# Kernel optimization log

Hardware: AMD Instinct MI355X
Metric: run time of the kernel (lower is better)

Reference implementation:

```python
import jax, jax.numpy as jnp
from jax import lax
import numpy as np

TAU = 10.0
BN_EPS = 1e-5
M_CENTROIDS = 1024
K_NEIGHBORS = 32


def fps(xyz, m):
    """Farthest point sampling for a single cloud xyz:(N,3) -> (m,) int32 indices."""
    N = xyz.shape[0]

    def step(carry, _):
        dists, last = carry
        d = jnp.sum((xyz - xyz[last]) ** 2, axis=-1)  # (N,)
        dists = jnp.minimum(dists, d)
        nxt = jnp.argmax(dists).astype(jnp.int32)
        return (dists, nxt), nxt

    init = (jnp.full((N,), 1e10, xyz.dtype), jnp.int32(0))
    _, idxs = lax.scan(step, init, None, length=m - 1)
    return jnp.concatenate([jnp.zeros((1,), jnp.int32), idxs])


def conv_bn_relu(x, W, g, b):
    # 1x1 Conv2d (no bias) == channel matmul; BatchNorm in train mode (batch stats)
    x = jnp.einsum('bmkc,oc->bmko', x, W)
    mu = jnp.mean(x, axis=(0, 1, 2))
    var = jnp.var(x, axis=(0, 1, 2))  # biased, matching torch BN normalization
    return jax.nn.relu((x - mu) * (g * lax.rsqrt(var + BN_EPS)) + b)


def lse_pool(x, tau=TAU):
    # Log-Sum-Exp pool over K axis (axis=2) of (B,M,K,C)
    x_max = jnp.max(x, axis=2)
    return x_max + jnp.log(jnp.sum(jnp.exp(tau * (x - x_max[:, :, None, :])), axis=2)) / tau


def setup_inputs() -> dict:
    key = jax.random.key(0)
    ks = jax.random.split(key, 5)
    B, N, C = 16, 4096, 64
    return {
        'xyz': jax.random.normal(ks[0], (B, N, 3), jnp.float32),
        'features': jax.random.normal(ks[1], (B, N, C), jnp.float32),
        'W1': jax.random.normal(ks[2], (64, 67), jnp.float32) * 0.1,
        'g1': jnp.ones((64,), jnp.float32),
        'b1': jnp.zeros((64,), jnp.float32),
        'W2': jax.random.normal(ks[3], (64, 64), jnp.float32) * 0.1,
        'g2': jnp.ones((64,), jnp.float32),
        'b2': jnp.zeros((64,), jnp.float32),
        'W3': jax.random.normal(ks[4], (128, 64), jnp.float32) * 0.1,
        'g3': jnp.ones((128,), jnp.float32),
        'b3': jnp.zeros((128,), jnp.float32),
    }


def reference(xyz, features, W1, g1, b1, W2, g2, b2, W3, g3, b3):
    B, N, _ = xyz.shape
    M, K = M_CENTROIDS, K_NEIGHBORS
    # FPS (indices non-differentiable, as in torch_geometric fps)
    idx = jax.vmap(lambda p: fps(p, M))(xyz)  # (B,M)
    centroids = jnp.take_along_axis(xyz, idx[:, :, None], axis=1)  # (B,M,3)
    # KNN via pairwise squared distances (computed under no_grad in original)
    d2 = (jnp.sum(centroids ** 2, -1)[:, :, None]
          + jnp.sum(xyz ** 2, -1)[:, None, :]
          - 2.0 * jnp.einsum('bmc,bnc->bmn', centroids, xyz))  # (B,M,N)
    group_idx = lax.top_k(-lax.stop_gradient(d2), K)[1]  # (B,M,K)
    bidx = jnp.arange(B)[:, None, None]
    grouped_xyz = xyz[bidx, group_idx] - centroids[:, :, None, :]  # (B,M,K,3)
    grouped_feat = features[bidx, group_idx]  # (B,M,K,C)
    x = jnp.concatenate([grouped_xyz, grouped_feat], axis=-1)  # (B,M,K,3+C)
    x = conv_bn_relu(x, W1, g1, b1)
    x = conv_bn_relu(x, W2, g2, b2)
    x = conv_bn_relu(x, W3, g3, b3)
    x = lse_pool(x)  # (B,M,128)
    return (centroids, x)
```

## Files before the change

kernel.cpp:

```cpp
#include <hip/hip_runtime.h>
#include <math.h>

#define B_   16
#define N_   4096
#define M_   1024
#define K_   32
#define CIN  67
#define NPOS (B_*M_*K_)
#define NBLK (NPOS/128)
#define BN_EPS 1e-5f

typedef unsigned short ushort_t;
typedef unsigned long long u64_t;

__device__ __forceinline__ unsigned int pack2bf(float a, float b) {
    unsigned int ua = __float_as_uint(a); ua = (ua + 0x7fffu + ((ua >> 16) & 1u)) >> 16;
    unsigned int ub = __float_as_uint(b); ub = (ub + 0x7fffu + ((ub >> 16) & 1u)) >> 16;
    return ua | (ub << 16);
}
__device__ __forceinline__ void unpack2(unsigned int u, float& lo, float& hi) {
    lo = __uint_as_float(u << 16);
    hi = __uint_as_float(u & 0xffff0000u);
}

__global__ __launch_bounds__(256) void fps_kernel(const float* __restrict__ xyz,
                                                  float* __restrict__ cent)
{
    __shared__ float sx[N_], sy[N_], sz[N_];
    __shared__ __align__(16) float red[2][4][8];
    const int b = blockIdx.x;
    const int t = threadIdx.x;

    const float4* xf = (const float4*)(xyz + (size_t)b * (N_*3));
#pragma unroll
    for (int u0 = 0; u0 < 4; ++u0) {
        const int u = u0 * 256 + t;
        const float4 q0 = xf[3*u+0], q1 = xf[3*u+1], q2 = xf[3*u+2];
        sx[4*u+0] = q0.x; sx[4*u+1] = q0.w; sx[4*u+2] = q1.z; sx[4*u+3] = q2.y;
        sy[4*u+0] = q0.y; sy[4*u+1] = q1.x; sy[4*u+2] = q1.w; sy[4*u+3] = q2.z;
        sz[4*u+0] = q0.z; sz[4*u+1] = q1.y; sz[4*u+2] = q2.x; sz[4*u+3] = q2.w;
    }
    __syncthreads();

    float px[16], py[16], pz[16], dist[16];
    unsigned int nl[16];
#pragma unroll
    for (int s = 0; s < 16; ++s) {
        const int p = s * 256 + t;
        px[s] = sx[p]; py[s] = sy[p]; pz[s] = sz[p];
        dist[s] = 1e10f;
        nl[s] = ~(unsigned int)p;
    }

    float cx = sx[0], cy = sy[0], cz = sz[0];
    if (t == 0) {
        float* o = cent + (size_t)b * M_ * 3;
        o[0] = cx; o[1] = cy; o[2] = cz;
    }
    const int lane = t & 63, w = t >> 6;

#pragma unroll 1
    for (int i = 1; i < M_; ++i) {
        u64_t best = 0ull;
#pragma unroll
        for (int s = 0; s < 16; ++s) {
            const float dx = __fsub_rn(px[s], cx);
            const float dy = __fsub_rn(py[s], cy);
            const float dz = __fsub_rn(pz[s], cz);
            const float d  = __fadd_rn(__fadd_rn(__fmul_rn(dx,dx), __fmul_rn(dy,dy)),
                                       __fmul_rn(dz,dz));
            dist[s] = fminf(dist[s], d);
            const u64_t cand = ((u64_t)__float_as_uint(dist[s]) << 32) | nl[s];
            best = (cand > best) ? cand : best;
        }
#pragma unroll
        for (int off = 32; off >= 1; off >>= 1) {
            const u64_t o = __shfl_down(best, off);
            best = (o > best) ? o : best;
        }
        if (lane == 0) {
            const unsigned int p = ~(unsigned int)(best & 0xffffffffull);
            red[i&1][w][0] = __uint_as_float((unsigned int)(best >> 32));
            red[i&1][w][1] = __uint_as_float((unsigned int)(best & 0xffffffffull));
            red[i&1][w][2] = sx[p]; red[i&1][w][3] = sy[p]; red[i&1][w][4] = sz[p];
        }
        __syncthreads();
        u64_t kk[4]; float xx[4], yy[4], zz[4];
#pragma unroll
        for (int ww = 0; ww < 4; ++ww) {
            const float4 r = *(const float4*)&red[i&1][ww][0];
            kk[ww] = ((u64_t)__float_as_uint(r.x) << 32) | __float_as_uint(r.y);
            xx[ww] = r.z; yy[ww] = r.w; zz[ww] = red[i&1][ww][4];
        }
#define MERGE_(a, c_) { const bool s_ = kk[c_] > kk[a]; \
        kk[a] = s_ ? kk[c_] : kk[a]; xx[a] = s_ ? xx[c_] : xx[a]; \
        yy[a] = s_ ? yy[c_] : yy[a]; zz[a] = s_ ? zz[c_] : zz[a]; }
        MERGE_(0,1); MERGE_(2,3); MERGE_(0,2);
#undef MERGE_
        cx = xx[0]; cy = yy[0]; cz = zz[0];
        if (t == 0) {
            float* o = cent + ((size_t)b * M_ + i) * 3;
            o[0] = cx; o[1] = cy; o[2] = cz;
        }
    }
}

__global__ __launch_bounds__(1024) void knn_kernel(const float* __restrict__ xyz,
                                                   const float* __restrict__ cent,
                                                   int* __restrict__ gidx)
{
    __shared__ float sx[N_], sy[N_], sz[N_], sn[N_];
    const int b  = blockIdx.x >> 6;
    const int mg = blockIdx.x & 63;
    const int t  = threadIdx.x;
    {
        const float4* xf = (const float4*)(xyz + (size_t)b * (N_*3));
        float4 q0 = xf[3*t+0], q1 = xf[3*t+1], q2 = xf[3*t+2];
        float ax[4] = {q0.x, q0.w, q1.z, q2.y};
        float ay[4] = {q0.y, q1.x, q1.w, q2.z};
        float az[4] = {q0.z, q1.y, q2.x, q2.w};
#pragma unroll
        for (int j = 0; j < 4; ++j) {
            const int p = 4*t + j;
            sx[p] = ax[j]; sy[p] = ay[j]; sz[p] = az[j];
            sn[p] = __fadd_rn(__fadd_rn(__fmul_rn(ax[j],ax[j]), __fmul_rn(ay[j],ay[j])),
                              __fmul_rn(az[j],az[j]));
        }
    }
    __syncthreads();
    const int w = t >> 6, lane = t & 63;
    const int m = mg * 16 + w;
    const float* c = cent + ((size_t)b * M_ + m) * 3;
    const float cx = c[0], cy = c[1], cz = c[2];
    const float cn = __fadd_rn(__fadd_rn(__fmul_rn(cx,cx), __fmul_rn(cy,cy)),
                               __fmul_rn(cz,cz));
    unsigned int key[64];
    u64_t b1 = ~0ull, b2 = ~0ull;
#pragma unroll
    for (int j = 0; j < 64; ++j) {
        const int p = j*64 + lane;
        const float dot = __fadd_rn(__fadd_rn(__fmul_rn(cx,sx[p]), __fmul_rn(cy,sy[p])),
                                    __fmul_rn(cz,sz[p]));
        const float d = __fsub_rn(__fadd_rn(cn, sn[p]), __fmul_rn(2.0f, dot));
        const unsigned int bb = __float_as_uint(d);
        const unsigned int k = (bb & 0x80000000u) ? ~bb : (bb | 0x80000000u);
        key[j] = k;
        const u64_t cand = ((u64_t)k << 32) | (unsigned int)p;
        if (cand < b1) { b2 = b1; b1 = cand; } else if (cand < b2) { b2 = cand; }
    }
    u64_t used = 0ull;
    int* gout = gidx + ((size_t)b * M_ + m) * K_;
#pragma unroll 1
    for (int r = 0; r < K_; ++r) {
        u64_t v = b1;
#pragma unroll
        for (int off = 1; off < 64; off <<= 1) {
            const u64_t ov = __shfl_xor(v, off);
            v = (ov < v) ? ov : v;
        }
        if (lane == 0) gout[r] = (int)(v & 0xffffffffull);
        if (v == b1) {
            const int p = (int)(v & 0xffffffffull);
            used |= (1ull << (p >> 6));
            if (b2 != ~0ull) { b1 = b2; b2 = ~0ull; }
            else {
                b1 = ~0ull; b2 = ~0ull;
#pragma unroll
                for (int jj = 0; jj < 64; ++jj) {
                    if (!(used & (1ull << jj))) {
                        const u64_t cand = ((u64_t)key[jj] << 32) | (unsigned int)(jj*64 + lane);
                        if (cand < b1) { b2 = b1; b1 = cand; } else if (cand < b2) { b2 = cand; }
                    }
                }
            }
        }
    }
}

__device__ __forceinline__ void write_stats64(float acc[4][8], float* part,
                                              float (*sred)[128][2], int t, int blk,
                                              int obase)
{
    const int lane = t & 63, w = t >> 6;
    const int txl = lane & 7, tyl = lane >> 3;
    float s[8], q[8];
#pragma unroll
    for (int j = 0; j < 8; ++j) {
        s[j] = ((acc[0][j] + acc[1][j]) + acc[2][j]) + acc[3][j];
        q[j] = ((acc[0][j]*acc[0][j] + acc[1][j]*acc[1][j]) + acc[2][j]*acc[2][j])
               + acc[3][j]*acc[3][j];
    }
#pragma unroll
    for (int off = 8; off < 64; off <<= 1) {
#pragma unroll
        for (int j = 0; j < 8; ++j) {
            s[j] += __shfl_xor(s[j], off);
            q[j] += __shfl_xor(q[j], off);
        }
    }
    if (tyl == 0) {
#pragma unroll
        for (int j = 0; j < 8; ++j) { sred[w][txl*8+j][0] = s[j]; sred[w][txl*8+j][1] = q[j]; }
    }
    __syncthreads();
    if (t < 128) {
        const int o = t >> 1, which = t & 1;
        const float v = ((sred[0][o][which] + sred[1][o][which]) + sred[2][o][which])
                        + sred[3][o][which];
        part[(size_t)(which*128 + obase + o) * NBLK + blk] = v;
    }
}

__device__ __forceinline__ void write_stats128(float a3[8][8], float* part,
                                               float (*sred)[128][2], int t, int blk)
{
    const int lane = t & 63, w = t >> 6;
    const int txl = lane & 15, tyl = lane >> 4;
    float s[8], q[8];
#pragma unroll
    for (int j = 0; j < 8; ++j) {
        float ss0 = 0.f, qq0 = 0.f;
#pragma unroll
        for (int i = 0; i < 8; ++i) { ss0 += a3[i][j]; qq0 += a3[i][j]*a3[i][j]; }
        s[j] = ss0; q[j] = qq0;
    }
#pragma unroll
    for (int off = 16; off < 64; off <<= 1) {
#pragma unroll
        for (int j = 0; j < 8; ++j) {
            s[j] += __shfl_xor(s[j], off);
            q[j] += __shfl_xor(q[j], off);
        }
    }
    if (tyl == 0) {
#pragma unroll
        for (int j = 0; j < 8; ++j) { sred[w][txl*8+j][0] = s[j]; sred[w][txl*8+j][1] = q[j]; }
    }
    __syncthreads();
    {
        const int o = t >> 1, which = t & 1;
        const float v = ((sred[0][o][which] + sred[1][o][which]) + sred[2][o][which])
                        + sred[3][o][which];
        part[(size_t)(which*128 + o) * NBLK + blk] = v;
    }
}

__global__ __launch_bounds__(256) void passA_kernel(const float* __restrict__ xyz,
    const float* __restrict__ feat, const float* __restrict__ W1,
    const float* __restrict__ cent, const int* __restrict__ gidx,
    float* __restrict__ part, ushort_t* __restrict__ z1)
{
    __shared__ __align__(16) float buf[CIN][132];
    __shared__ __align__(16) float wb[64*68];
    __shared__ float sred[4][128][2];
    const int t = threadIdx.x;
    const int blk = blockIdx.x;
    const int pos0 = blk * 128;

    {
        const int ph = t >> 1, half = t & 1;
        const int pos = pos0 + ph;
        const int b = pos >> 15;
        const int n = gidx[pos];
        const float* fbase = feat + ((((size_t)b << 12) + (size_t)n) << 6) + (half << 5);
        const float4* fp4 = (const float4*)fbase;
#pragma unroll
        for (int q = 0; q < 8; ++q) {
            const float4 v = fp4[q];
            const int c = 3 + (half << 5) + (q << 2);
            buf[c+0][ph] = v.x; buf[c+1][ph] = v.y; buf[c+2][ph] = v.z; buf[c+3][ph] = v.w;
        }
        if (half == 0) {
            const int bm = pos >> 5;
            const float* pp = xyz + (((size_t)b << 12) + (size_t)n) * 3;
            const float* cc = cent + (size_t)bm * 3;
            buf[0][ph] = __fsub_rn(pp[0], cc[0]);
            buf[1][ph] = __fsub_rn(pp[1], cc[1]);
            buf[2][ph] = __fsub_rn(pp[2], cc[2]);
        }
        const int o = t & 63, chunk = t >> 6;
        const int c0 = chunk * 17;
        const int c1 = (c0 + 17 < CIN) ? (c0 + 17) : CIN;
        for (int c = c0; c < c1; ++c) wb[c*68 + o] = W1[o*CIN + c];
    }
    __syncthreads();

    const int tx = t & 7, ty = t >> 3;
    float acc[4][8];
#pragma unroll
    for (int i = 0; i < 4; ++i)
#pragma unroll
        for (int j = 0; j < 8; ++j) acc[i][j] = 0.0f;
#pragma unroll 1
    for (int c = 0; c < CIN; ++c) {
        const float4 xv = *(const float4*)&buf[c][ty*4];
        const float4 w0 = *(const float4*)&wb[c*68 + tx*8];
        const float4 w1 = *(const float4*)&wb[c*68 + tx*8 + 4];
        const float xs[4] = {xv.x, xv.y, xv.z, xv.w};
        const float wv[8] = {w0.x, w0.y, w0.z, w0.w, w1.x, w1.y, w1.z, w1.w};
#pragma unroll
        for (int i = 0; i < 4; ++i)
#pragma unroll
            for (int j = 0; j < 8; ++j) acc[i][j] = fmaf(xs[i], wv[j], acc[i][j]);
    }
    write_stats64(acc, part, sred, t, blk, 0);
#pragma unroll
    for (int i = 0; i < 4; ++i) {
        uint4 s;
        s.x = pack2bf(acc[i][0], acc[i][1]); s.y = pack2bf(acc[i][2], acc[i][3]);
        s.z = pack2bf(acc[i][4], acc[i][5]); s.w = pack2bf(acc[i][6], acc[i][7]);
        *(uint4*)(z1 + ((size_t)(pos0 + ty*4 + i)) * 64 + tx*8) = s;
    }
}

__global__ __launch_bounds__(256) void passB_kernel(const float* __restrict__ W2,
    const float* __restrict__ ss, const ushort_t* __restrict__ z1,
    float* __restrict__ part, ushort_t* __restrict__ z2)
{
    __shared__ __align__(16) float buf[64][132];
    __shared__ __align__(16) float wb[64*68];
    __shared__ float sred[4][128][2];
    __shared__ float ssl[64], ssh[64];
    const int t = threadIdx.x;
    const int blk = blockIdx.x;
    const int pos0 = blk * 128;

    if (t < 64) { ssl[t] = ss[t]; ssh[t] = ss[128 + t]; }
    {
        const int o = t & 63, chunk = t >> 6;
#pragma unroll
        for (int cc2 = 0; cc2 < 16; ++cc2) {
            const int c = chunk*16 + cc2;
            wb[c*68 + o] = W2[o*64 + c];
        }
    }
    __syncthreads();

    {
        const int ph = t >> 1, half = t & 1;
        const uint4* zr = (const uint4*)(z1 + ((size_t)(pos0 + ph)) * 64 + half*32);
#pragma unroll
        for (int q = 0; q < 4; ++q) {
            const uint4 r = zr[q];
            const int c = half*32 + q*8;
            float lo, hi;
            unpack2(r.x, lo, hi);
            buf[c+0][ph] = fmaxf(fmaf(lo, ssl[c+0], ssh[c+0]), 0.f);
            buf[c+1][ph] = fmaxf(fmaf(hi, ssl[c+1], ssh[c+1]), 0.f);
            unpack2(r.y, lo, hi);
            buf[c+2][ph] = fmaxf(fmaf(lo, ssl[c+2], ssh[c+2]), 0.f);
            buf[c+3][ph] = fmaxf(fmaf(hi, ssl[c+3], ssh[c+3]), 0.f);
            unpack2(r.z, lo, hi);
            buf[c+4][ph] = fmaxf(fmaf(lo, ssl[c+4], ssh[c+4]), 0.f);
            buf[c+5][ph] = fmaxf(fmaf(hi, ssl[c+5], ssh[c+5]), 0.f);
            unpack2(r.w, lo, hi);
            buf[c+6][ph] = fmaxf(fmaf(lo, ssl[c+6], ssh[c+6]), 0.f);
            buf[c+7][ph] = fmaxf(fmaf(hi, ssl[c+7], ssh[c+7]), 0.f);
        }
    }
    __syncthreads();

    const int tx = t & 7, ty = t >> 3;
    float acc[4][8];
#pragma unroll
    for (int i = 0; i < 4; ++i)
#pragma unroll
        for (int j = 0; j < 8; ++j) acc[i][j] = 0.0f;
#pragma unroll 1
    for (int c = 0; c < 64; ++c) {
        const float4 xv = *(const float4*)&buf[c][ty*4];
        const float4 w0 = *(const float4*)&wb[c*68 + tx*8];
        const float4 w1 = *(const float4*)&wb[c*68 + tx*8 + 4];
        const float xs[4] = {xv.x, xv.y, xv.z, xv.w};
        const float wv[8] = {w0.x, w0.y, w0.z, w0.w, w1.x, w1.y, w1.z, w1.w};
#pragma unroll
        for (int i = 0; i < 4; ++i)
#pragma unroll
            for (int j = 0; j < 8; ++j) acc[i][j] = fmaf(xs[i], wv[j], acc[i][j]);
    }
    write_stats64(acc, part, sred, t, blk, 0);
#pragma unroll
    for (int i = 0; i < 4; ++i) {
        uint4 s;
        s.x = pack2bf(acc[i][0], acc[i][1]); s.y = pack2bf(acc[i][2], acc[i][3]);
        s.z = pack2bf(acc[i][4], acc[i][5]); s.w = pack2bf(acc[i][6], acc[i][7]);
        *(uint4*)(z2 + ((size_t)(pos0 + ty*4 + i)) * 64 + tx*8) = s;
    }
}

__global__ __launch_bounds__(256) void passC_kernel(const float* __restrict__ W3,
    const float* __restrict__ ss, const ushort_t* __restrict__ z2,
    float* __restrict__ part, ushort_t* __restrict__ z3)
{
    __shared__ __align__(16) float buf[64][132];
    __shared__ __align__(16) float wb[64*68];
    __shared__ float sred[4][128][2];
    __shared__ float ssl[64], ssh[64];
    const int t = threadIdx.x;
    const int blk = blockIdx.x;
    const int pos0 = blk * 128;

    if (t < 64) { ssl[t] = ss[256 + t]; ssh[t] = ss[384 + t]; }
    {
        const int o = t & 63, chunk = t >> 6;
#pragma unroll
        for (int cc3 = 0; cc3 < 16; ++cc3) {
            const int c = chunk*16 + cc3;
            wb[c*68 + o] = W3[o*64 + c];
        }
    }
    __syncthreads();

    {
        const int ph = t >> 1, half = t & 1;
        const uint4* zr = (const uint4*)(z2 + ((size_t)(pos0 + ph)) * 64 + half*32);
#pragma unroll
        for (int q = 0; q < 4; ++q) {
            const uint4 r = zr[q];
            const int c = half*32 + q*8;
            float lo, hi;
            unpack2(r.x, lo, hi);
            buf[c+0][ph] = fmaxf(fmaf(lo, ssl[c+0], ssh[c+0]), 0.f);
            buf[c+1][ph] = fmaxf(fmaf(hi, ssl[c+1], ssh[c+1]), 0.f);
            unpack2(r.y, lo, hi);
            buf[c+2][ph] = fmaxf(fmaf(lo, ssl[c+2], ssh[c+2]), 0.f);
            buf[c+3][ph] = fmaxf(fmaf(hi, ssl[c+3], ssh[c+3]), 0.f);
            unpack2(r.z, lo, hi);
            buf[c+4][ph] = fmaxf(fmaf(lo, ssl[c+4], ssh[c+4]), 0.f);
            buf[c+5][ph] = fmaxf(fmaf(hi, ssl[c+5], ssh[c+5]), 0.f);
            unpack2(r.w, lo, hi);
            buf[c+6][ph] = fmaxf(fmaf(lo, ssl[c+6], ssh[c+6]), 0.f);
            buf[c+7][ph] = fmaxf(fmaf(hi, ssl[c+7], ssh[c+7]), 0.f);
        }
    }
    __syncthreads();

    const int tx = t & 7, ty = t >> 3;
#pragma unroll 1
    for (int h = 0; h < 2; ++h) {
        float acc[4][8];
#pragma unroll
        for (int i = 0; i < 4; ++i)
#pragma unroll
            for (int j = 0; j < 8; ++j) acc[i][j] = 0.0f;
#pragma unroll 1
        for (int c = 0; c < 64; ++c) {
            const float4 xv = *(const float4*)&buf[c][ty*4];
            const float4 w0 = *(const float4*)&wb[c*68 + tx*8];
            const float4 w1 = *(const float4*)&wb[c*68 + tx*8 + 4];
            const float xs[4] = {xv.x, xv.y, xv.z, xv.w};
            const float wv[8] = {w0.x, w0.y, w0.z, w0.w, w1.x, w1.y, w1.z, w1.w};
#pragma unroll
            for (int i = 0; i < 4; ++i)
#pragma unroll
                for (int j = 0; j < 8; ++j) acc[i][j] = fmaf(xv[i], wv[j], acc[i][j]);
        }
        write_stats64(acc, part, sred, t, blk, h*64);
#pragma unroll
        for (int i = 0; i < 4; ++i) {
            uint4 s;
            s.x = pack2bf(acc[i][0], acc[i][1]); s.y = pack2bf(acc[i][2], acc[i][3]);
            s.z = pack2bf(acc[i][4], acc[i][5]); s.w = pack2bf(acc[i][6], acc[i][7]);
            *(uint4*)(z3 + ((size_t)(pos0 + ty*4 + i)) * 128 + h*64 + tx*8) = s;
        }
        if (h == 0) {
            const int o = t & 63, chunk = t >> 6;
#pragma unroll
            for (int cc3 = 0; cc3 < 16; ++cc3) {
                const int c = chunk*16 + cc3;
                wb[c*68 + o] = W3[(64 + o)*64 + c];
            }
            __syncthreads();
        }
    }
}

__global__ __launch_bounds__(256) void passD_kernel(const float* __restrict__ ss,
    const ushort_t* __restrict__ z3, float* __restrict__ outx)
{
    const int t = threadIdx.x;
    const int blk = blockIdx.x;
    const int pos0 = blk * 128;
    const int tx3 = t & 15, ty3 = t >> 4;
    const int lane = t & 63, w = t >> 6;
    float scl[8], shf[8];
#pragma unroll
    for (int j = 0; j < 8; ++j) { scl[j] = ss[512 + tx3*8 + j]; shf[j] = ss[640 + tx3*8 + j]; }

    float v[8][8];
#pragma unroll
    for (int i = 0; i < 8; ++i) {
        const uint4 r = *(const uint4*)(z3 + ((size_t)(pos0 + ty3*8 + i)) * 128 + tx3*8);
        float lo, hi;
        unpack2(r.x, lo, hi);
        v[i][0] = fmaxf(fmaf(lo, scl[0], shf[0]), 0.f);
        v[i][1] = fmaxf(fmaf(hi, scl[1], shf[1]), 0.f);
        unpack2(r.y, lo, hi);
        v[i][2] = fmaxf(fmaf(lo, scl[2], shf[2]), 0.f);
        v[i][3] = fmaxf(fmaf(hi, scl[3], shf[3]), 0.f);
        unpack2(r.z, lo, hi);
        v[i][4] = fmaxf(fmaf(lo, scl[4], shf[4]), 0.f);
        v[i][5] = fmaxf(fmaf(hi, scl[5], shf[5]), 0.f);
        unpack2(r.w, lo, hi);
        v[i][6] = fmaxf(fmaf(lo, scl[6], shf[6]), 0.f);
        v[i][7] = fmaxf(fmaf(hi, scl[7], shf[7]), 0.f);
    }
    float mrow[8], srow[8];
#pragma unroll
    for (int j = 0; j < 8; ++j) {
        float mm = v[0][j];
#pragma unroll
        for (int i = 1; i < 8; ++i) mm = fmaxf(mm, v[i][j]);
        float sm = 0.0f;
#pragma unroll
        for (int i = 0; i < 8; ++i) sm += expf(10.0f * (v[i][j] - mm));
        mrow[j] = mm; srow[j] = sm;
    }
#pragma unroll
    for (int off = 16; off <= 32; off <<= 1) {
#pragma unroll
        for (int j = 0; j < 8; ++j) {
            const float om = __shfl_xor(mrow[j], off);
            const float os = __shfl_xor(srow[j], off);
            const float nm = fmaxf(mrow[j], om);
            srow[j] = srow[j] * expf(10.0f*(mrow[j]-nm)) + os * expf(10.0f*(om-nm));
            mrow[j] = nm;
        }
    }
    if ((lane >> 4) == 0) {
        const int bm = blk*4 + w;
#pragma unroll
        for (int j = 0; j < 8; ++j)
            outx[(size_t)bm*128 + tx3*8 + j] = mrow[j] + logf(srow[j]) / 10.0f;
    }
}

template<int PASS>
__global__ __launch_bounds__(256) void fwd_kernel(const float* __restrict__ xyz,
    const float* __restrict__ feat, const float* __restrict__ W1,
    const float* __restrict__ W2, const float* __restrict__ W3,
    const float* __restrict__ cent, const int* __restrict__ gidx,
    const float* __restrict__ ss, float* __restrict__ part, float* __restrict__ outx)
{
    __shared__ __align__(16) float buf[CIN][132];
    __shared__ __align__(16) float wb[64*132];
    __shared__ float sred[4][128][2];
    const int t = threadIdx.x;
    const int blk = blockIdx.x;
    const int pos0 = blk * 128;
    const int lane = t & 63, w = t >> 6;

    {
        const int ph = t >> 1, half = t & 1;
        const int pos = pos0 + ph;
        const int b = pos >> 15;
        const int n = gidx[pos];
        const float* fbase = feat + ((((size_t)b << 12) + (size_t)n) << 6) + (half << 5);
        const float4* fp4 = (const float4*)fbase;
#pragma unroll
        for (int q = 0; q < 8; ++q) {
            const float4 v = fp4[q];
            const int c = 3 + (half << 5) + (q << 2);
            buf[c+0][ph] = v.x; buf[c+1][ph] = v.y; buf[c+2][ph] = v.z; buf[c+3][ph] = v.w;
        }
        if (half == 0) {
            const int bm = pos >> 5;
            const float* pp = xyz + (((size_t)b << 12) + (size_t)n) * 3;
            const float* cc = cent + (size_t)bm * 3;
            buf[0][ph] = __fsub_rn(pp[0], cc[0]);
            buf[1][ph] = __fsub_rn(pp[1], cc[1]);
            buf[2][ph] = __fsub_rn(pp[2], cc[2]);
        }
        const int o = t & 63, chunk = t >> 6;
        const int c0 = chunk * 17;
        const int c1 = (c0 + 17 < CIN) ? (c0 + 17) : CIN;
        for (int c = c0; c < c1; ++c) wb[c*68 + o] = W1[o*CIN + c];
    }
    __syncthreads();

    const int tx = t & 7, ty = t >> 3;
    float acc[4][8];
#pragma unroll
    for (int i = 0; i < 4; ++i)
#pragma unroll
        for (int j = 0; j < 8; ++j) acc[i][j] = 0.0f;
#pragma unroll 1
    for (int c = 0; c < CIN; ++c) {
        const float4 xv = *(const float4*)&buf[c][ty*4];
        const float4 w0 = *(const float4*)&wb[c*68 + tx*8];
        const float4 w1 = *(const float4*)&wb[c*68 + tx*8 + 4];
        const float xs[4] = {xv.x, xv.y, xv.z, xv.w};
        const float wv[8] = {w0.x, w0.y, w0.z, w0.w, w1.x, w1.y, w1.z, w1.w};
#pragma unroll
        for (int i = 0; i < 4; ++i)
#pragma unroll
            for (int j = 0; j < 8; ++j) acc[i][j] = fmaf(xs[i], wv[j], acc[i][j]);
    }
    if (PASS == 1) { write_stats64(acc, part, sred, t, blk, 0); return; }

    __syncthreads();
    {
        float scl[8], shf[8];
#pragma unroll
        for (int j = 0; j < 8; ++j) { scl[j] = ss[tx*8+j]; shf[j] = ss[128 + tx*8+j]; }
#pragma unroll
        for (int jj = 0; jj < 8; ++jj) {
            const int j = (tx + jj) & 7;
#pragma unroll
            for (int i = 0; i < 4; ++i)
                buf[tx*8+j][ty*4+i] = fmaxf(fmaf(acc[i][j], scl[j], shf[j]), 0.0f);
        }
        const int o = t & 63, chunk = t >> 6;
#pragma unroll
        for (int cc2 = 0; cc2 < 16; ++cc2) {
            const int c = chunk*16 + cc2;
            wb[c*68 + o] = W2[o*64 + c];
        }
    }
    __syncthreads();

#pragma unroll
    for (int i = 0; i < 4; ++i)
#pragma unroll
        for (int j = 0; j < 8; ++j) acc[i][j] = 0.0f;
#pragma unroll 1
    for (int c = 0; c < 64; ++c) {
        const float4 xv = *(const float4*)&buf[c][ty*4];
        const float4 w0 = *(const float4*)&wb[c*68 + tx*8];
        const float4 w1 = *(const float4*)&wb[c*68 + tx*8 + 4];
        const float xs[4] = {xv.x, xv.y, xv.z, xv.w};
        const float wv[8] = {w0.x, w0.y, w0.z, w0.w, w1.x, w1.y, w1.z, w1.w};
#pragma unroll
        for (int i = 0; i < 4; ++i)
#pragma unroll
            for (int j = 0; j < 8; ++j) acc[i][j] = fmaf(xs[i], wv[j], acc[i][j]);
    }
    if (PASS == 2) { write_stats64(acc, part, sred, t, blk, 0); return; }

    __syncthreads();
    {
        float scl[8], shf[8];
#pragma unroll
        for (int j = 0; j < 8; ++j) { scl[j] = ss[256 + tx*8+j]; shf[j] = ss[256 + 128 + tx*8+j]; }
#pragma unroll
        for (int jj = 0; jj < 8; ++jj) {
            const int j = (tx + jj) & 7;
#pragma unroll
            for (int i = 0; i < 4; ++i)
                buf[tx*8+j][ty*4+i] = fmaxf(fmaf(acc[i][j], scl[j], shf[j]), 0.0f);
        }
        const int o = t & 127, chunk = t >> 7;
#pragma unroll
        for (int cc3 = 0; cc3 < 32; ++cc3) {
            const int c = chunk*32 + cc3;
            wb[c*132 + o] = W3[o*64 + c];
        }
    }
    __syncthreads();

    const int tx3 = t & 15, ty3 = t >> 4;
    float a3[8][8];
#pragma unroll
    for (int i = 0; i < 8; ++i)
#pragma unroll
        for (int j = 0; j < 8; ++j) a3[i][j] = 0.0f;
#pragma unroll 1
    for (int c = 0; c < 64; ++c) {
        const float4 x0 = *(const float4*)&buf[c][ty3*8];
        const float4 x1 = *(const float4*)&buf[c][ty3*8 + 4];
        const float4 w0 = *(const float4*)&wb[c*132 + tx3*8];
        const float4 w1 = *(const float4*)&wb[c*132 + tx3*8 + 4];
        const float xs[8] = {x0.x, x0.y, x0.z, x0.w, x1.x, x1.y, x1.z, x1.w};
        const float wv[8] = {w0.x, w0.y, w0.z, w0.w, w1.x, w1.y, w1.z, w1.w};
#pragma unroll
        for (int i = 0; i < 8; ++i)
#pragma unroll
            for (int j = 0; j < 8; ++j) a3[i][j] = fmaf(xs[i], wv[j], a3[i][j]);
    }
    if (PASS == 3) { write_stats128(a3, part, sred, t, blk); return; }

    {
        float scl[8], shf[8];
#pragma unroll
        for (int j = 0; j < 8; ++j) { scl[j] = ss[512 + tx3*8+j]; shf[j] = ss[512 + 128 + tx3*8+j]; }
        float mrow[8], srow[8];
#pragma unroll
        for (int j = 0; j < 8; ++j) {
            float vv[8];
#pragma unroll
            for (int i = 0; i < 8; ++i)
                vv[i] = fmaxf(fmaf(a3[i][j], scl[j], shf[j]), 0.0f);
            float mm = vv[0];
#pragma unroll
            for (int i = 1; i < 8; ++i) mm = fmaxf(mm, vv[i]);
            float sm = 0.0f;
#pragma unroll
            for (int i = 0; i < 8; ++i) sm += expf(10.0f * (vv[i] - mm));
            mrow[j] = mm; srow[j] = sm;
        }
#pragma unroll
        for (int off = 16; off <= 32; off <<= 1) {
#pragma unroll
            for (int j = 0; j < 8; ++j) {
                const float om = __shfl_xor(mrow[j], off);
                const float os = __shfl_xor(srow[j], off);
                const float nm = fmaxf(mrow[j], om);
                srow[j] = srow[j] * expf(10.0f*(mrow[j]-nm)) + os * expf(10.0f*(om-nm));
                mrow[j] = nm;
            }
        }
        if ((lane >> 4) == 0) {
            const int bm = blk*4 + w;
#pragma unroll
            for (int j = 0; j < 8; ++j)
                outx[(size_t)bm*128 + tx3*8 + j] = mrow[j] + logf(srow[j]) / 10.0f;
        }
    }
}

__global__ __launch_bounds__(256) void stats_kernel(const float* __restrict__ part,
    const float* __restrict__ g, const float* __restrict__ bet,
    float* __restrict__ ss, int si)
{
    __shared__ float red[512];
    const int o = blockIdx.x, t = threadIdx.x;
    const float* ps = part + (size_t)o * NBLK;
    const float* pq = part + (size_t)(128 + o) * NBLK;
    float s = 0.0f, q = 0.0f;
    for (int i = t; i < NBLK; i += 256) { s += ps[i]; q += pq[i]; }
    red[t] = s; red[256 + t] = q;
    __syncthreads();
    for (int st = 128; st > 0; st >>= 1) {
        if (t < st) { red[t] += red[t + st]; red[256+t] += red[256+t+st]; }
        __syncthreads();
    }
    if (t == 0) {
        const float inv = 1.0f / (float)NPOS;
        const float mu  = red[0] * inv;
        const float var = red[256] * inv - mu * mu;
        const float scale = g[o] / sqrtf(var + BN_EPS);
        ss[si*256 + o]       = scale;
        ss[si*256 + 128 + o] = bet[o] - mu * scale;
    }
}

extern "C" void kernel_launch(void* const* d_in, const int* in_sizes, int n_in,
                              void* d_out, int out_size, void* d_ws, size_t ws_size,
                              hipStream_t stream) {
    const float* xyz  = (const float*)d_in[0];
    const float* feat = (const float*)d_in[1];
    const float* W1   = (const float*)d_in[2];
    const float* g1   = (const float*)d_in[3];
    const float* b1   = (const float*)d_in[4];
    const float* W2   = (const float*)d_in[5];
    const float* g2   = (const float*)d_in[6];
    const float* b2   = (const float*)d_in[7];
    const float* W3   = (const float*)d_in[8];
    const float* g3   = (const float*)d_in[9];
    const float* b3   = (const float*)d_in[10];
    float* out = (float*)d_out;
    float* wsf = (float*)d_ws;

    float* part = wsf;
    int*   gidx = (int*)(wsf + 2*128*NBLK);
    float* ss   = wsf + 2*128*NBLK + NPOS;
    float* outx = out + B_*M_*3;

    const size_t BASE0 = (size_t)(2*128*NBLK + NPOS + 768) * 4;
    const size_t ZA_BYTES = (size_t)NPOS * 128 * 2;
    const size_t ZB_BYTES = (size_t)NPOS * 64 * 2;
    const size_t NEED = BASE0 + ZA_BYTES + ZB_BYTES;
    ushort_t* zA = (ushort_t*)((char*)d_ws + BASE0);
    ushort_t* zB = (ushort_t*)((char*)d_ws + BASE0 + ZA_BYTES);

    fps_kernel<<<dim3(B_), dim3(256), 0, stream>>>(xyz, out);
    knn_kernel<<<dim3(B_*64), dim3(1024), 0, stream>>>(xyz, out, gidx);

    if (ws_size >= NEED) {
        passA_kernel<<<dim3(NBLK), dim3(256), 0, stream>>>(xyz, feat, W1, out, gidx, part, zA);
        stats_kernel<<<dim3(64), dim3(256), 0, stream>>>(part, g1, b1, ss, 0);
        passB_kernel<<<dim3(NBLK), dim3(256), 0, stream>>>(W2, ss, zA, part, zB);
        stats_kernel<<<dim3(64), dim3(256), 0, stream>>>(part, g2, b2, ss, 1);
        passC_kernel<<<dim3(NBLK), dim3(256), 0, stream>>>(W3, ss, zB, part, zA);
        stats_kernel<<<dim3(128), dim3(256), 0, stream>>>(part, g3, b3, ss, 2);
        passD_kernel<<<dim3(NBLK), dim3(256), 0, stream>>>(ss, zA, outx);
    } else {
        fwd_kernel<1><<<dim3(NBLK), dim3(256), 0, stream>>>(xyz, feat, W1, W2, W3, out, gidx, ss, part, outx);
        stats_kernel<<<dim3(64), dim3(256), 0, stream>>>(part, g1, b1, ss, 0);
        fwd_kernel<2><<<dim3(NBLK), dim3(256), 0, stream>>>(xyz, feat, W1, W2, W3, out, gidx, ss, part, outx);
        stats_kernel<<<dim3(64), dim3(256), 0, stream>>>(part, g2, b2, ss, 1);
        fwd_kernel<3><<<dim3(NBLK), dim3(256), 0, stream>>>(xyz, feat, W1, W2, W3, out, gidx, ss, part, outx);
        stats_kernel<<<dim3(128), dim3(256), 0, stream>>>(part, g3, b3, ss, 2);
        fwd_kernel<4><<<dim3(NBLK), dim3(256), 0, stream>>>(xyz, feat, W1, W2, W3, out, gidx, ss, part, outx);
    }
}
```

Before: 1.666 ms.

## Precompute per-point feature projection and overlap it with FPS blocks

The first 1x1 conv is split algebraically. The 64 feature channels are projected once per input point (B*N points instead of B*M*K grouped positions), and only the 3 relative-xyz channels are applied per neighbour in passA, which gathers the precomputed rows. That projection runs as extra blocks inside the FPS launch so it overlaps the long serial FPS loop. FPS now reduces only indices per step and writes centroids at the end, and passC computes all 128 outputs in one pass with a padded weight tile. The fp32 projected buffer reuses the zB workspace, and the larger shared-memory footprint of the combined kernel may reduce occupancy.

Result: faster. 1.483 ms (-11.0%).

```diff
diff --git a/kernel.cpp b/kernel.cpp
--- a/kernel.cpp
+++ b/kernel.cpp
@@ -23,84 +23,126 @@
     hi = __uint_as_float(u & 0xffff0000u);
 }
 
-__global__ __launch_bounds__(256) void fps_kernel(const float* __restrict__ xyz,
-                                                  float* __restrict__ cent)
+__global__ __launch_bounds__(256) void fps_a0_kernel(const float* __restrict__ xyz,
+    float* __restrict__ cent, const float* __restrict__ feat,
+    const float* __restrict__ W1, float* __restrict__ z1u)
 {
     __shared__ float sx[N_], sy[N_], sz[N_];
-    __shared__ __align__(16) float red[2][4][8];
-    const int b = blockIdx.x;
+    __shared__ u64_t red[2][4];
+    __shared__ int cidx[M_];
+    __shared__ __align__(16) float buf[64][132];
+    __shared__ __align__(16) float wb[64*68];
+
     const int t = threadIdx.x;
 
-    const float4* xf = (const float4*)(xyz + (size_t)b * (N_*3));
-#pragma unroll
-    for (int u0 = 0; u0 < 4; ++u0) {
-        const int u = u0 * 256 + t;
-        const float4 q0 = xf[3*u+0], q1 = xf[3*u+1], q2 = xf[3*u+2];
-        sx[4*u+0] = q0.x; sx[4*u+1] = q0.w; sx[4*u+2] = q1.z; sx[4*u+3] = q2.y;
-        sy[4*u+0] = q0.y; sy[4*u+1] = q1.x; sy[4*u+2] = q1.w; sy[4*u+3] = q2.z;
-        sz[4*u+0] = q0.z; sz[4*u+1] = q1.y; sz[4*u+2] = q2.x; sz[4*u+3] = q2.w;
-    }
-    __syncthreads();
-
-    float px[16], py[16], pz[16], dist[16];
-    unsigned int nl[16];
-#pragma unroll
-    for (int s = 0; s < 16; ++s) {
-        const int p = s * 256 + t;
-        px[s] = sx[p]; py[s] = sy[p]; pz[s] = sz[p];
-        dist[s] = 1e10f;
-        nl[s] = ~(unsigned int)p;
-    }
-
-    float cx = sx[0], cy = sy[0], cz = sz[0];
-    if (t == 0) {
-        float* o = cent + (size_t)b * M_ * 3;
-        o[0] = cx; o[1] = cy; o[2] = cz;
-    }
-    const int lane = t & 63, w = t >> 6;
-
+    if (blockIdx.x < 16) {
+        const int b = blockIdx.x;
+        const float4* xf = (const float4*)(xyz + (size_t)b * (N_*3));
+#pragma unroll
+        for (int u0 = 0; u0 < 4; ++u0) {
+            const int u = u0 * 256 + t;
+            const float4 q0 = xf[3*u+0], q1 = xf[3*u+1], q2 = xf[3*u+2];
+            sx[4*u+0] = q0.x; sx[4*u+1] = q0.w; sx[4*u+2] = q1.z; sx[4*u+3] = q2.y;
+            sy[4*u+0] = q0.y; sy[4*u+1] = q1.x; sy[4*u+2] = q1.w; sy[4*u+3] = q2.z;
+            sz[4*u+0] = q0.z; sz[4*u+1] = q1.y; sz[4*u+2] = q2.x; sz[4*u+3] = q2.w;
+        }
+        if (t == 0) cidx[0] = 0;
+        __syncthreads();
+
+        float px[16], py[16], pz[16], dist[16];
+        unsigned int nl[16];
+#pragma unroll
+        for (int s = 0; s < 16; ++s) {
+            const int p = s * 256 + t;
+            px[s] = sx[p]; py[s] = sy[p]; pz[s] = sz[p];
+            dist[s] = 1e10f;
+            nl[s] = ~(unsigned int)p;
+        }
+
+        int last = 0;
 #pragma unroll 1
-    for (int i = 1; i < M_; ++i) {
-        u64_t best = 0ull;
-#pragma unroll
-        for (int s = 0; s < 16; ++s) {
-            const float dx = __fsub_rn(px[s], cx);
-            const float dy = __fsub_rn(py[s], cy);
-            const float dz = __fsub_rn(pz[s], cz);
-            const float d  = __fadd_rn(__fadd_rn(__fmul_rn(dx,dx), __fmul_rn(dy,dy)),
-                                       __fmul_rn(dz,dz));
-            dist[s] = fminf(dist[s], d);
-            const u64_t cand = ((u64_t)__float_as_uint(dist[s]) << 32) | nl[s];
-            best = (cand > best) ? cand : best;
-        }
-#pragma unroll
-        for (int off = 32; off >= 1; off >>= 1) {
-            const u64_t o = __shfl_down(best, off);
-            best = (o > best) ? o : best;
-        }
-        if (lane == 0) {
-            const unsigned int p = ~(unsigned int)(best & 0xffffffffull);
-            red[i&1][w][0] = __uint_as_float((unsigned int)(best >> 32));
-            red[i&1][w][1] = __uint_as_float((unsigned int)(best & 0xffffffffull));
-            red[i&1][w][2] = sx[p]; red[i&1][w][3] = sy[p]; red[i&1][w][4] = sz[p];
+        for (int i = 1; i < M_; ++i) {
+            const float cx = sx[last], cy = sy[last], cz = sz[last];
+            u64_t best = 0ull;
+#pragma unroll
+            for (int s = 0; s < 16; ++s) {
+                const float dx = __fsub_rn(px[s], cx);
+                const float dy = __fsub_rn(py[s], cy);
+                const float dz = __fsub_rn(pz[s], cz);
+                const float d  = __fadd_rn(__fadd_rn(__fmul_rn(dx,dx), __fmul_rn(dy,dy)),
+                                           __fmul_rn(dz,dz));
+                dist[s] = fminf(dist[s], d);
+                const u64_t cand = ((u64_t)__float_as_uint(dist[s]) << 32) | nl[s];
+                best = (cand > best) ? cand : best;
+            }
+#pragma unroll
+            for (int off = 1; off < 64; off <<= 1) {
+                const u64_t o = __shfl_xor(best, off);
+                best = (o > best) ? o : best;
+            }
+            if ((t & 63) == 0) red[i & 1][t >> 6] = best;
+            __syncthreads();
+            const u64_t g0 = red[i&1][0], g1 = red[i&1][1];
+            const u64_t g2 = red[i&1][2], g3 = red[i&1][3];
+            const u64_t ga = (g0 > g1) ? g0 : g1;
+            const u64_t gb = (g2 > g3) ? g2 : g3;
+            const u64_t g  = (ga > gb) ? ga : gb;
+            last = (int)(~(unsigned int)g);
+            if (t == 0) cidx[i] = last;
         }
         __syncthreads();
-        u64_t kk[4]; float xx[4], yy[4], zz[4];
-#pragma unroll
-        for (int ww = 0; ww < 4; ++ww) {
-            const float4 r = *(const float4*)&red[i&1][ww][0];
-            kk[ww] = ((u64_t)__float_as_uint(r.x) << 32) | __float_as_uint(r.y);
-            xx[ww] = r.z; yy[ww] = r.w; zz[ww] = red[i&1][ww][4];
-        }
-#define MERGE_(a, c_) { const bool s_ = kk[c_] > kk[a]; \
-        kk[a] = s_ ? kk[c_] : kk[a]; xx[a] = s_ ? xx[c_] : xx[a]; \
-        yy[a] = s_ ? yy[c_] : yy[a]; zz[a] = s_ ? zz[c_] : zz[a]; }
-        MERGE_(0,1); MERGE_(2,3); MERGE_(0,2);
-#undef MERGE_
-        cx = xx[0]; cy = yy[0]; cz = zz[0];
-        if (t == 0) {
-            float* o = cent + ((size_t)b * M_ + i) * 3;
-            o[0] = cx; o[1] = cy; o[2] = cz;
+#pragma unroll
+        for (int u0 = 0; u0 < 4; ++u0) {
+            const int u = u0 * 256 + t;
+            const int ci = cidx[u];
+            float* o = cent + ((size_t)b * M_ + u) * 3;
+            o[0] = sx[ci]; o[1] = sy[ci]; o[2] = sz[ci];
+        }
+    } else {
+        const int blk = blockIdx.x - 16;
+        const int pos0 = blk * 128;
+        {
+            const int ph = t >> 1, half = t & 1;
+            const int pos = pos0 + ph;
+            const float4* fp4 = (const float4*)(feat + ((size_t)pos << 6) + (half << 5));
+#pragma unroll
+            for (int q = 0; q < 8; ++q) {
+                const float4 v = fp4[q];
+                const int c = (half << 5) + (q << 2);
+                buf[c+0][ph] = v.x; buf[c+1][ph] = v.y; buf[c+2][ph] = v.z; buf[c+3][ph] = v.w;
+            }
+            const int o = t & 63, chunk = t >> 6;
+#pragma unroll
+            for (int cc = 0; cc < 16; ++cc) {
+                const int c = chunk*16 + cc;
+                wb[c*68 + o] = W1[o*CIN + 3 + c];
+            }
+        }
+        __syncthreads();
+
+        const int tx = t & 7, ty = t >> 3;
+        float acc[4][8];
+#pragma unroll
+        for (int i = 0; i < 4; ++i)
+#pragma unroll
+            for (int j = 0; j < 8; ++j) acc[i][j] = 0.0f;
+#pragma unroll 1
+        for (int c = 0; c < 64; ++c) {
+            const float4 xv = *(const float4*)&buf[c][ty*4];
+            const float4 w0 = *(const float4*)&wb[c*68 + tx*8];
+            const float4 w1 = *(const float4*)&wb[c*68 + tx*8 + 4];
+            const float xs[4] = {xv.x, xv.y, xv.z, xv.w};
+            const float wv[8] = {w0.x, w0.y, w0.z, w0.w, w1.x, w1.y, w1.z, w1.w};
+#pragma unroll
+            for (int i = 0; i < 4; ++i)
+#pragma unroll
+                for (int j = 0; j < 8; ++j) acc[i][j] = fmaf(xs[i], wv[j], acc[i][j]);
+        }
+#pragma unroll
+        for (int i = 0; i < 4; ++i) {
+            float* zp = z1u + ((size_t)(pos0 + ty*4 + i)) * 64 + tx*8;
+            *(float4*)zp       = make_float4(acc[i][0], acc[i][1], acc[i][2], acc[i][3]);
+            *(float4*)(zp + 4) = make_float4(acc[i][4], acc[i][5], acc[i][6], acc[i][7]);
         }
     }
 }
@@ -246,62 +288,59 @@
 }
 
 __global__ __launch_bounds__(256) void passA_kernel(const float* __restrict__ xyz,
-    const float* __restrict__ feat, const float* __restrict__ W1,
     const float* __restrict__ cent, const int* __restrict__ gidx,
+    const float* __restrict__ W1, const float* __restrict__ z1u,
     float* __restrict__ part, ushort_t* __restrict__ z1)
 {
-    __shared__ __align__(16) float buf[CIN][132];
-    __shared__ __align__(16) float wb[64*68];
+    __shared__ float rel[3][132];
+    __shared__ int   sn_[132];
+    __shared__ float wx[3*64];
     __shared__ float sred[4][128][2];
     const int t = threadIdx.x;
     const int blk = blockIdx.x;
     const int pos0 = blk * 128;
 
-    {
-        const int ph = t >> 1, half = t & 1;
+    if (t < 128) {
+        const int pos = pos0 + t;
+        const int b = pos >> 15;
+        const int n = gidx[pos];
+        const int bm = pos >> 5;
+        const float* pp = xyz + (((size_t)b << 12) + (size_t)n) * 3;
+        const float* cc = cent + (size_t)bm * 3;
+        rel[0][t] = __fsub_rn(pp[0], cc[0]);
+        rel[1][t] = __fsub_rn(pp[1], cc[1]);
+        rel[2][t] = __fsub_rn(pp[2], cc[2]);
+        sn_[t] = n;
+    } else if (t < 128 + 64) {
+        const int o = t - 128;
+        wx[0*64 + o] = W1[o*CIN + 0];
+        wx[1*64 + o] = W1[o*CIN + 1];
+        wx[2*64 + o] = W1[o*CIN + 2];
+    }
+    __syncthreads();
+
+    const int tx = t & 7, ty = t >> 3;
+    float w0r[8], w1r[8], w2r[8];
+#pragma unroll
+    for (int j = 0; j < 8; ++j) {
+        w0r[j] = wx[0*64 + tx*8 + j];
+        w1r[j] = wx[1*64 + tx*8 + j];
+        w2r[j] = wx[2*64 + tx*8 + j];
+    }
+    float acc[4][8];
+#pragma unroll
+    for (int i = 0; i < 4; ++i) {
+        const int ph = ty*4 + i;
         const int pos = pos0 + ph;
         const int b = pos >> 15;
-        const int n = gidx[pos];
-        const float* fbase = feat + ((((size_t)b << 12) + (size_t)n) << 6) + (half << 5);
-        const float4* fp4 = (const float4*)fbase;
-#pragma unroll
-        for (int q = 0; q < 8; ++q) {
-            const float4 v = fp4[q];
-            const int c = 3 + (half << 5) + (q << 2);
-            buf[c+0][ph] = v.x; buf[c+1][ph] = v.y; buf[c+2][ph] = v.z; buf[c+3][ph] = v.w;
-        }
-        if (half == 0) {
-            const int bm = pos >> 5;
-            const float* pp = xyz + (((size_t)b << 12) + (size_t)n) * 3;
-            const float* cc = cent + (size_t)bm * 3;
-            buf[0][ph] = __fsub_rn(pp[0], cc[0]);
-            buf[1][ph] = __fsub_rn(pp[1], cc[1]);
-            buf[2][ph] = __fsub_rn(pp[2], cc[2]);
-        }
-        const int o = t & 63, chunk = t >> 6;
-        const int c0 = chunk * 17;
-        const int c1 = (c0 + 17 < CIN) ? (c0 + 17) : CIN;
-        for (int c = c0; c < c1; ++c) wb[c*68 + o] = W1[o*CIN + c];
-    }
-    __syncthreads();
-
-    const int tx = t & 7, ty = t >> 3;
-    float acc[4][8];
-#pragma unroll
-    for (int i = 0; i < 4; ++i)
-#pragma unroll
-        for (int j = 0; j < 8; ++j) acc[i][j] = 0.0f;
-#pragma unroll 1
-    for (int c = 0; c < CIN; ++c) {
-        const float4 xv = *(const float4*)&buf[c][ty*4];
-        const float4 w0 = *(const float4*)&wb[c*68 + tx*8];
-        const float4 w1 = *(const float4*)&wb[c*68 + tx*8 + 4];
-        const float xs[4] = {xv.x, xv.y, xv.z, xv.w};
-        const float wv[8] = {w0.x, w0.y, w0.z, w0.w, w1.x, w1.y, w1.z, w1.w};
-#pragma unroll
-        for (int i = 0; i < 4; ++i)
-#pragma unroll
-            for (int j = 0; j < 8; ++j) acc[i][j] = fmaf(xs[i], wv[j], acc[i][j]);
+        const size_t idx = ((size_t)b << 12) + (size_t)sn_[ph];
+        const float4 f0 = *(const float4*)(z1u + idx*64 + tx*8);
+        const float4 f1 = *(const float4*)(z1u + idx*64 + tx*8 + 4);
+        const float fp[8] = {f0.x, f0.y, f0.z, f0.w, f1.x, f1.y, f1.z, f1.w};
+        const float r0 = rel[0][ph], r1 = rel[1][ph], r2 = rel[2][ph];
+#pragma unroll
+        for (int j = 0; j < 8; ++j)
+            acc[i][j] = fmaf(r2, w2r[j], fmaf(r1, w1r[j], fmaf(r0, w0r[j], fp[j])));
     }
     write_stats64(acc, part, sred, t, blk, 0);
 #pragma unroll
@@ -393,7 +432,7 @@
     float* __restrict__ part, ushort_t* __restrict__ z3)
 {
     __shared__ __align__(16) float buf[64][132];
-    __shared__ __align__(16) float wb[64*68];
+    __shared__ __align__(16) float wbC[64*140];
     __shared__ float sred[4][128][2];
     __shared__ float ssl[64], ssh[64];
     const int t = threadIdx.x;
@@ -402,11 +441,12 @@
 
     if (t < 64) { ssl[t] = ss[256 + t]; ssh[t] = ss[384 + t]; }
     {
-        const int o = t & 63, chunk = t >> 6;
-#pragma unroll
-        for (int cc3 = 0; cc3 < 16; ++cc3) {
-            const int c = chunk*16 + cc3;
-            wb[c*68 + o] = W3[o*64 + c];
+        const int o = t & 127, chunk = t >> 7;
+        const int pad = o + 4*(o >> 5);
+#pragma unroll
+        for (int cc = 0; cc < 32; ++cc) {
+            const int c = chunk*32 + cc;
+            wbC[c*140 + pad] = W3[o*64 + c];
         }
     }
     __syncthreads();
@@ -435,43 +475,33 @@
     }
     __syncthreads();
 
-    const int tx = t & 7, ty = t >> 3;
+    const int tx3 = t & 15, ty3 = t >> 4;
+    const int opad = tx3*8 + 4*(tx3 >> 2);
+    float a3[8][8];
+#pragma unroll
+    for (int i = 0; i < 8; ++i)
+#pragma unroll
+        for (int j = 0; j < 8; ++j) a3[i][j] = 0.0f;
 #pragma unroll 1
-    for (int h = 0; h < 2; ++h) {
-        float acc[4][8];
-#pragma unroll
-        for (int i = 0; i < 4; ++i)
-#pragma unroll
-            for (int j = 0; j < 8; ++j) acc[i][j] = 0.0f;
-#pragma unroll 1
-        for (int c = 0; c < 64; ++c) {
-            const float4 xv = *(const float4*)&buf[c][ty*4];
-            const float4 w0 = *(const float4*)&wb[c*68 + tx*8];
-            const float4 w1 = *(const float4*)&wb[c*68 + tx*8 + 4];
-            const float xs[4] = {xv.x, xv.y, xv.z, xv.w};
-            const float wv[8] = {w0.x, w0.y, w0.z, w0.w, w1.x, w1.y, w1.z, w1.w};
-#pragma unroll
-            for (int i = 0; i < 4; ++i)
-#pragma unroll
-                for (int j = 0; j < 8; ++j) acc[i][j] = fmaf(xv[i], wv[j], acc[i][j]);
-        }
-        write_stats64(acc, part, sred, t, blk, h*64);
-#pragma unroll
-        for (int i = 0; i < 4; ++i) {
-            uint4 s;
-            s.x = pack2bf(acc[i][0], acc[i][1]); s.y = pack2bf(acc[i][2], acc[i][3]);
-            s.z = pack2bf(acc[i][4], acc[i][5]); s.w = pack2bf(acc[i][6], acc[i][7]);
-            *(uint4*)(z3 + ((size_t)(pos0 + ty*4 + i)) * 128 + h*64 + tx*8) = s;
-        }
-        if (h == 0) {
-            const int o = t & 63, chunk = t >> 6;
-#pragma unroll
-            for (int cc3 = 0; cc3 < 16; ++cc3) {
-                const int c = chunk*16 + cc3;
-                wb[c*68 + o] = W3[(64 + o)*64 + c];
-            }
-            __syncthreads();
-        }
+    for (int c = 0; c < 64; ++c) {
+        const float4 x0 = *(const float4*)&buf[c][ty3*8];
+        const float4 x1 = *(const float4*)&buf[c][ty3*8 + 4];
+        const float4 w0 = *(const float4*)&wbC[c*140 + opad];
+        const float4 w1 = *(const float4*)&wbC[c*140 + opad + 4];
+        const float xs[8] = {x0.x, x0.y, x0.z, x0.w, x1.x, x1.y, x1.z, x1.w};
+        const float wv[8] = {w0.x, w0.y, w0.z, w0.w, w1.x, w1.y, w1.z, w1.w};
+#pragma unroll
+        for (int i = 0; i < 8; ++i)
+#pragma unroll
+            for (int j = 0; j < 8; ++j) a3[i][j] = fmaf(xs[i], wv[j], a3[i][j]);
+    }
+    write_stats128(a3, part, sred, t, blk);
+#pragma unroll
+    for (int i = 0; i < 8; ++i) {
+        uint4 s;
+        s.x = pack2bf(a3[i][0], a3[i][1]); s.y = pack2bf(a3[i][2], a3[i][3]);
+        s.z = pack2bf(a3[i][4], a3[i][5]); s.w = pack2bf(a3[i][6], a3[i][7]);
+        *(uint4*)(z3 + ((size_t)(pos0 + ty3*8 + i)) * 128 + tx3*8) = s;
     }
 }
 
@@ -772,12 +802,13 @@
     const size_t NEED = BASE0 + ZA_BYTES + ZB_BYTES;
     ushort_t* zA = (ushort_t*)((char*)d_ws + BASE0);
     ushort_t* zB = (ushort_t*)((char*)d_ws + BASE0 + ZA_BYTES);
-
-    fps_kernel<<<dim3(B_), dim3(256), 0, stream>>>(xyz, out);
-    knn_kernel<<<dim3(B_*64), dim3(1024), 0, stream>>>(xyz, out, gidx);
+    float*    z1u = (float*)zB;
 
     if (ws_size >= NEED) {
-        passA_kernel<<<dim3(NBLK), dim3(256), 0, stream>>>(xyz, feat, W1, out, gidx, part, zA);
+        fps_a0_kernel<<<dim3(16 + 512), dim3(256), 0, stream>>>(xyz, out, feat, W1, z1u);
+        knn_kernel<<<dim3(B_*64), dim3(1024), 0, stream>>>(xyz, out, gidx);
+
+        passA_kernel<<<dim3(NBLK), dim3(256), 0, stream>>>(xyz, out, gidx, W1, z1u, part, zA);
         stats_kernel<<<dim3(64), dim3(256), 0, stream>>>(part, g1, b1, ss, 0);
         passB_kernel<<<dim3(NBLK), dim3(256), 0, stream>>>(W2, ss, zA, part, zB);
         stats_kernel<<<dim3(64), dim3(256), 0, stream>>>(part, g2, b2, ss, 1);
@@ -785,6 +816,9 @@
         stats_kernel<<<dim3(128), dim3(256), 0, stream>>>(part, g3, b3, ss, 2);
         passD_kernel<<<dim3(NBLK), dim3(256), 0, stream>>>(ss, zA, outx);
     } else {
+        fps_a0_kernel<<<dim3(16), dim3(256), 0, stream>>>(xyz, out, feat, W1, (float*)0);
+        knn_kernel<<<dim3(B_*64), dim3(1024), 0, stream>>>(xyz, out, gidx);
+
         fwd_kernel<1><<<dim3(NBLK), dim3(256), 0, stream>>>(xyz, feat, W1, W2, W3, out, gidx, ss, part, outx);
         stats_kernel<<<dim3(64), dim3(256), 0, stream>>>(part, g1, b1, ss, 0);
         fwd_kernel<2><<<dim3(NBLK), dim3(256), 0, stream>>>(xyz, feat, W1, W2, W3, out, gidx, ss, part, outx);
```
